# Kernel optimization log

Measured on AMD Instinct MI355X. Metric: run time of the kernel, lower is better.

## Reference

```python
import jax, jax.numpy as jnp
import numpy as np

N, E, IN, H, ED, G, OUT = 50000, 800000, 128, 256, 32, 500, 16
LN_EPS = 1e-5
BN_EPS = 1e-5


def _w(key, shape, scale=0.05):
    return scale * jax.random.normal(key, shape, dtype=jnp.float32)


def setup_inputs() -> dict:
    key = jax.random.key(0)
    ks = iter(jax.random.split(key, 64))
    inp = {
        'x': jax.random.normal(next(ks), (N, IN), jnp.float32),
        'edge_index': jax.random.randint(next(ks), (2, E), 0, N, jnp.int64),
        'edge_attr': jax.random.normal(next(ks), (E, ED), jnp.float32),
        'batch': jnp.sort(jax.random.randint(next(ks), (N,), 0, G, jnp.int64)),
    }
    def conv_params(pfx, din):
        return {
            pfx + '_Wq': _w(next(ks), (din, H)), pfx + '_bq': jnp.zeros((H,), jnp.float32),
            pfx + '_Wk': _w(next(ks), (din, H)), pfx + '_bk': jnp.zeros((H,), jnp.float32),
            pfx + '_Wv': _w(next(ks), (din, H)), pfx + '_bv': jnp.zeros((H,), jnp.float32),
            pfx + '_We': _w(next(ks), (ED, H)),
            pfx + '_Ws': _w(next(ks), (din, H)), pfx + '_bs': jnp.zeros((H,), jnp.float32),
        }
    inp.update(conv_params('conv1', IN))
    inp.update({'ln1_g': jnp.ones((H,), jnp.float32), 'ln1_b': jnp.zeros((H,), jnp.float32)})
    inp.update(conv_params('conv2', H))
    inp.update({'ln2_g': jnp.ones((H,), jnp.float32), 'ln2_b': jnp.zeros((H,), jnp.float32)})
    for pfx in ('gin1', 'gin2'):
        inp.update({
            pfx + '_W1': _w(next(ks), (H, H)), pfx + '_b1': jnp.zeros((H,), jnp.float32),
            pfx + '_bng': jnp.ones((H,), jnp.float32), pfx + '_bnb': jnp.zeros((H,), jnp.float32),
            pfx + '_W2': _w(next(ks), (H, H)), pfx + '_b2': jnp.zeros((H,), jnp.float32),
        })
    inp.update({'lin_W': _w(next(ks), (H, H)), 'lin_b': jnp.zeros((H,), jnp.float32),
                'clf_W': _w(next(ks), (H, OUT)), 'clf_b': jnp.zeros((OUT,), jnp.float32)})
    return inp


def transformer_conv(x, src, dst, ea, Wq, bq, Wk, bk, Wv, bv, We, Ws, bs):
    # PyG TransformerConv, heads=1, edge_dim set, root_weight=True, beta=False
    h = Wq.shape[1]
    q = x @ Wq + bq                      # [N,H]
    e = ea @ We                          # [E,H]
    ke = (x @ Wk + bk)[src] + e          # [E,H]
    ve = (x @ Wv + bv)[src] + e          # [E,H]
    score = jnp.sum(q[dst] * ke, axis=-1) / jnp.sqrt(jnp.float32(h))  # [E]
    m = jax.ops.segment_max(score, dst, num_segments=N)
    ex = jnp.exp(score - m[dst])
    denom = jax.ops.segment_sum(ex, dst, num_segments=N)
    alpha = ex / (denom[dst] + 1e-16)
    out = jax.ops.segment_sum(alpha[:, None] * ve, dst, num_segments=N)
    return out + x @ Ws + bs


def layer_norm(x, g, b):
    mu = jnp.mean(x, axis=-1, keepdims=True)
    var = jnp.var(x, axis=-1, keepdims=True)
    return (x - mu) * jax.lax.rsqrt(var + LN_EPS) * g + b


def gin_conv(x, src, dst, W1, b1, bng, bnb, W2, b2):
    # GINConv(eps=0): mlp(x + sum_{j in N(i)} x_j); MLP = Linear-BN-ReLU-Linear
    agg = jax.ops.segment_sum(x[src], dst, num_segments=N)
    h = x + agg
    y = h @ W1 + b1
    mu = jnp.mean(y, axis=0)
    var = jnp.var(y, axis=0)
    y = (y - mu) * jax.lax.rsqrt(var + BN_EPS) * bng + bnb
    y = jax.nn.relu(y)
    return y @ W2 + b2


def reference(x, edge_index, edge_attr, batch,
              conv1_Wq, conv1_bq, conv1_Wk, conv1_bk, conv1_Wv, conv1_bv, conv1_We, conv1_Ws, conv1_bs,
              ln1_g, ln1_b,
              conv2_Wq, conv2_bq, conv2_Wk, conv2_bk, conv2_Wv, conv2_bv, conv2_We, conv2_Ws, conv2_bs,
              ln2_g, ln2_b,
              gin1_W1, gin1_b1, gin1_bng, gin1_bnb, gin1_W2, gin1_b2,
              gin2_W1, gin2_b1, gin2_bng, gin2_bnb, gin2_W2, gin2_b2,
              lin_W, lin_b, clf_W, clf_b):
    src, dst = edge_index[0], edge_index[1]
    # NodeEncoder (dropout inactive in eval)
    h = transformer_conv(x, src, dst, edge_attr, conv1_Wq, conv1_bq, conv1_Wk, conv1_bk,
                         conv1_Wv, conv1_bv, conv1_We, conv1_Ws, conv1_bs)
    h = layer_norm(jax.nn.leaky_relu(h), ln1_g, ln1_b)
    h = transformer_conv(h, src, dst, edge_attr, conv2_Wq, conv2_bq, conv2_Wk, conv2_bk,
                         conv2_Wv, conv2_bv, conv2_We, conv2_Ws, conv2_bs)
    h = layer_norm(jax.nn.leaky_relu(h), ln2_g, ln2_b)
    # GIN_Net, max_depth=2: conv -> relu -> conv
    h = gin_conv(h, src, dst, gin1_W1, gin1_b1, gin1_bng, gin1_bnb, gin1_W2, gin1_b2)
    h = jax.nn.relu(h)
    h = gin_conv(h, src, dst, gin2_W1, gin2_b1, gin2_bng, gin2_bnb, gin2_W2, gin2_b2)
    # global_add_pool + MLP head
    pooled = jax.ops.segment_sum(h, batch, num_segments=G)   # [G,H]
    z = jax.nn.relu(pooled @ lin_W + lin_b)
    return z @ clf_W + clf_b                                 # [G,OUT]
```

## Files before the change

### kernel.cpp

```cpp
#include <hip/hip_runtime.h>
#include <math.h>

#define NN 50000
#define NE 800000
#define DIN 128
#define DH 256
#define DED 32
#define NG 500
#define DOUT 16
#define SCAN_T 256

typedef __bf16 bf16_t;
typedef __bf16 bf16x4 __attribute__((ext_vector_type(4)));
typedef __bf16 bf16x8 __attribute__((ext_vector_type(8)));
typedef float f32x4 __attribute__((ext_vector_type(4)));

__device__ __forceinline__ void async_copy16(const bf16_t* g, bf16_t* l) {
  __builtin_amdgcn_global_load_lds(
      (const __attribute__((address_space(1))) void*)g,
      (__attribute__((address_space(3))) void*)l, 16, 0, 0);
}

__global__ void fill_i32(int* __restrict__ p, int v, int n) {
  int i = blockIdx.x * 256 + threadIdx.x;
  if (i < n) p[i] = v;
}
__global__ void cast_bf16_k(const float* __restrict__ in, bf16_t* __restrict__ o, long n) {
  long i = (long)blockIdx.x * 256 + threadIdx.x;
  if (i < n) o[i] = (bf16_t)in[i];
}

__global__ void count_k(const int* __restrict__ dst, int* __restrict__ deg) {
  int e = blockIdx.x * 256 + threadIdx.x;
  if (e < NE) atomicAdd(&deg[dst[e]], 1);
}
__global__ void scan1(const int* __restrict__ deg, int* __restrict__ rowptr,
                      int* __restrict__ bsum, int n) {
  __shared__ int s[SCAN_T];
  int t = threadIdx.x, i = blockIdx.x * SCAN_T + t;
  int v = (i < n) ? deg[i] : 0;
  s[t] = v; __syncthreads();
  for (int off = 1; off < SCAN_T; off <<= 1) {
    int add = (t >= off) ? s[t - off] : 0;
    __syncthreads(); s[t] += add; __syncthreads();
  }
  if (i < n) rowptr[i + 1] = s[t];
  if (t == SCAN_T - 1) bsum[blockIdx.x] = s[t];
}
__global__ void scan2(const int* __restrict__ bsum, int* __restrict__ boff, int nb) {
  __shared__ int s[SCAN_T];
  int t = threadIdx.x;
  int v = (t < nb) ? bsum[t] : 0;
  s[t] = v; __syncthreads();
  for (int off = 1; off < SCAN_T; off <<= 1) {
    int add = (t >= off) ? s[t - off] : 0;
    __syncthreads(); s[t] += add; __syncthreads();
  }
  boff[t] = s[t] - v;
}
__global__ void scan3(int* __restrict__ rowptr, const int* __restrict__ boff, int n) {
  int i = blockIdx.x * 256 + threadIdx.x;
  if (i < n) rowptr[i + 1] += boff[i >> 8];
  if (i == 0) rowptr[0] = 0;
}
__global__ void scatter_k(const int* __restrict__ dst, const int* __restrict__ src,
                          const int* __restrict__ rowptr, int* __restrict__ cursor,
                          int* __restrict__ esrc, int* __restrict__ epos) {
  int e = blockIdx.x * 256 + threadIdx.x;
  if (e < NE) {
    int d = dst[e];
    int pos = rowptr[d] + atomicAdd(&cursor[d], 1);
    esrc[pos] = src[e];
    epos[e] = pos;
  }
}
__global__ void permute_ea(const int* __restrict__ epos, const float* __restrict__ ea,
                           bf16_t* __restrict__ eac) {
  long t = (long)blockIdx.x * 256 + threadIdx.x;
  if (t >= (long)NE * 4) return;
  int e = (int)(t >> 2), c8 = ((int)t & 3) * 8;
  int pos = epos[e];
  const float* sp = &ea[(size_t)e * DED + c8];
  bf16x8 o;
#pragma unroll
  for (int j = 0; j < 8; ++j) o[j] = (bf16_t)sp[j];
  *(bf16x8*)&eac[(size_t)pos * DED + c8] = o;
}

struct PackEnt { const float* src; bf16_t* dst; int K; int N; };
struct PackArgs { PackEnt e[16]; };
__global__ void pack_all(PackArgs pa) {
  PackEnt en = pa.e[blockIdx.y];
  int i = blockIdx.x * 256 + threadIdx.x;
  if (i >= en.K * en.N) return;
  int el = i & 511, f = i >> 9;
  int ntiles = en.N >> 4;
  int ks = f / ntiles, t = f - ks * ntiles;
  int lane = el >> 3, j = el & 7;
  int k = ks * 32 + (lane >> 4) * 8 + j;
  int n = t * 16 + (lane & 15);
  en.dst[i] = (bf16_t)en.src[(size_t)k * en.N + n];
}

__global__ void wqe_k(const float* __restrict__ Wq, const float* __restrict__ We,
                      const float* __restrict__ bq, float* __restrict__ Wqe,
                      float* __restrict__ bqe, int din) {
  int idx = blockIdx.x * 256 + threadIdx.x;
  if (idx < din * 32) {
    int d = idx >> 5, j = idx & 31;
    float s = 0.f;
    for (int h = 0; h < DH; ++h) s += Wq[(size_t)d * DH + h] * We[(size_t)j * DH + h];
    Wqe[idx] = s;
  }
  if (idx < 32) {
    float s = 0.f;
    for (int h = 0; h < DH; ++h) s += bq[h] * We[(size_t)idx * DH + h];
    bqe[idx] = s;
  }
}

template<int NT, int RT>
__device__ __forceinline__ void gemm_body(
    const bf16_t* __restrict__ Ab, const bf16_t* __restrict__ Wp,
    const float* __restrict__ bias, float* __restrict__ Cf, bf16_t* __restrict__ Cb,
    int M, int K, int relu, int rstride, int bx,
    float* __restrict__ psum, float* __restrict__ psq)
{
  __shared__ bf16_t Atile[RT * 2048];
  __shared__ bf16_t Btile[NT * 512];
  int tid = threadIdx.x;
  int lane = tid & 63, wv = tid >> 6;
  int base = bx * (RT * 64);
  f32x4 acc[RT][NT];
#pragma unroll
  for (int rt = 0; rt < RT; ++rt)
#pragma unroll
    for (int t = 0; t < NT; ++t) acc[rt][t] = (f32x4){0.f, 0.f, 0.f, 0.f};
  int arow = wv * (16 * RT) + (lane & 15);
  int aq = (lane >> 4) * 8;
  int nk = K >> 5;
  const int ACH = RT * 256;
  const int NCH = ACH + NT * 64;
  for (int ks = 0; ks < nk; ++ks) {
    __syncthreads();
    for (int c = tid; c < NCH; c += 256) {
      if (c < ACH) {
        int r = c >> 2, q = c & 3;
        async_copy16(Ab + (size_t)(base + r) * K + ks * 32 + q * 8, &Atile[c * 8]);
      } else {
        int cb = c - ACH;
        async_copy16(Wp + (size_t)ks * NT * 512 + cb * 8, &Btile[cb * 8]);
      }
    }
    __syncthreads();
    bf16x8 a[RT];
#pragma unroll
    for (int rt = 0; rt < RT; ++rt)
      a[rt] = *(const bf16x8*)&Atile[(arow + rt * 16) * 32 + aq];
#pragma unroll
    for (int t = 0; t < NT; ++t) {
      bf16x8 b = *(const bf16x8*)&Btile[t * 512 + lane * 8];
#pragma unroll
      for (int rt = 0; rt < RT; ++rt)
        acc[rt][t] = __builtin_amdgcn_mfma_f32_16x16x32_bf16(a[rt], b, acc[rt][t], 0, 0, 0);
    }
  }
  int col_l = lane & 15;
#pragma unroll
  for (int rt = 0; rt < RT; ++rt) {
    int rbase = base + wv * (16 * RT) + rt * 16 + (lane >> 4) * 4;
#pragma unroll
    for (int t = 0; t < NT; ++t) {
      int col = t * 16 + col_l;
      float bv = bias ? bias[col] : 0.f;
#pragma unroll
      for (int r = 0; r < 4; ++r) {
        int row = rbase + r;
        if (row >= M) continue;
        float vv = acc[rt][t][r] + bv;
        if (relu) vv = fmaxf(vv, 0.f);
        if (Cf) Cf[(size_t)row * rstride + col] = vv;
        if (Cb) Cb[(size_t)row * rstride + col] = (bf16_t)vv;
      }
    }
  }
  if (psum) {
#pragma unroll
    for (int t = 0; t < NT; ++t) {
      float sc = 0.f, sq = 0.f;
      float bv = bias[t * 16 + col_l];
#pragma unroll
      for (int rt = 0; rt < RT; ++rt) {
        int rbase = base + wv * (16 * RT) + rt * 16 + (lane >> 4) * 4;
#pragma unroll
        for (int r = 0; r < 4; ++r) {
          if (rbase + r >= M) continue;
          float vv = acc[rt][t][r] + bv;
          sc += vv; sq += vv * vv;
        }
      }
      sc += __shfl_xor(sc, 16, 64); sc += __shfl_xor(sc, 32, 64);
      sq += __shfl_xor(sq, 16, 64); sq += __shfl_xor(sq, 32, 64);
      if (lane < 16) {
        int col = t * 16 + lane;
        atomicAdd(&psum[wv * DH + col], sc);
        atomicAdd(&psq[wv * DH + col], sq);
      }
    }
  }
}

template<int NT>
__global__ __launch_bounds__(256, 3) void gemm_r1(
    const bf16_t* __restrict__ Ab, const bf16_t* __restrict__ Wp,
    const float* __restrict__ bias, float* __restrict__ Cf, bf16_t* __restrict__ Cb,
    int M, int K, int relu, int rstride, float* psum, float* psq)
{
  gemm_body<NT, 1>(Ab, Wp, bias, Cf, Cb, M, K, relu, rstride, blockIdx.x, psum, psq);
}

struct QkvsArgs { const bf16_t* w[4]; const float* bias[4]; bf16_t* outp[4]; };
__global__ __launch_bounds__(256, 3) void gemm_qkvs(
    const bf16_t* __restrict__ Ab, QkvsArgs qa, int M, int K)
{
  int which = blockIdx.y;
  gemm_body<16, 2>(Ab, qa.w[which], qa.bias[which], nullptr, qa.outp[which], M, K, 0, 1024,
                   blockIdx.x, nullptr, nullptr);
}

__global__ __launch_bounds__(256) void conv_edge_fused(
    const int* __restrict__ rowptr, const int* __restrict__ esrc,
    const bf16_t* __restrict__ qkvs, const bf16_t* __restrict__ eac,
    const float* __restrict__ QEf,
    bf16_t* __restrict__ AGGn, bf16_t* __restrict__ EAn)
{
  int half = threadIdx.x >> 5, l = threadIdx.x & 31;
  int n = blockIdx.x * 8 + half;
  if (n >= NN) return;
  float q[8];
  {
    bf16x8 t = *(const bf16x8*)&qkvs[(size_t)n * 1024 + l * 8];
#pragma unroll
    for (int j = 0; j < 8; ++j) q[j] = (float)t[j];
  }
  float qe[8];
#pragma unroll
  for (int j = 0; j < 8; ++j) qe[j] = 0.f;
  if (l < 4) {
    const float* p = &QEf[(size_t)n * DED + l * 8];
#pragma unroll
    for (int j = 0; j < 8; ++j) qe[j] = p[j];
  }
  float s = 0.f;
  float acc[8], eacc[8];
#pragma unroll
  for (int j = 0; j < 8; ++j) { acc[j] = 0.f; eacc[j] = 0.f; }
  int i0 = rowptr[n], i1 = rowptr[n + 1];
  for (int wb = i0; wb < i1; wb += 32) {
    int wcnt = min(32, i1 - wb);
    int widx = (l < wcnt) ? esrc[wb + l] : 0;
    int e = 0;
    for (; e + 4 <= wcnt; e += 4) {
      int s1 = __shfl(widx, e, 32);
      int s2 = __shfl(widx, e + 1, 32);
      int s3 = __shfl(widx, e + 2, 32);
      int s4 = __shfl(widx, e + 3, 32);
      const bf16_t* b1 = &qkvs[(size_t)s1 * 1024 + 256 + l * 8];
      const bf16_t* b2 = &qkvs[(size_t)s2 * 1024 + 256 + l * 8];
      const bf16_t* b3 = &qkvs[(size_t)s3 * 1024 + 256 + l * 8];
      const bf16_t* b4 = &qkvs[(size_t)s4 * 1024 + 256 + l * 8];
      bf16x8 k1 = *(const bf16x8*)b1;
      bf16x8 k2 = *(const bf16x8*)b2;
      bf16x8 k3 = *(const bf16x8*)b3;
      bf16x8 k4 = *(const bf16x8*)b4;
      bf16x8 v1 = *(const bf16x8*)(b1 + 256);
      bf16x8 v2 = *(const bf16x8*)(b2 + 256);
      bf16x8 v3 = *(const bf16x8*)(b3 + 256);
      bf16x8 v4 = *(const bf16x8*)(b4 + 256);
      bf16x8 t1 = {}, t2 = {}, t3 = {}, t4 = {};
      if (l < 4) {
        const bf16_t* ep = &eac[(size_t)(wb + e) * DED + l * 8];
        t1 = *(const bf16x8*)ep;
        t2 = *(const bf16x8*)(ep + DED);
        t3 = *(const bf16x8*)(ep + 2 * DED);
        t4 = *(const bf16x8*)(ep + 3 * DED);
      }
      float p1 = 0.f, p2 = 0.f, p3 = 0.f, p4 = 0.f;
#pragma unroll
      for (int j = 0; j < 8; ++j) {
        p1 = fmaf(q[j], (float)k1[j], p1);
        p2 = fmaf(q[j], (float)k2[j], p2);
        p3 = fmaf(q[j], (float)k3[j], p3);
        p4 = fmaf(q[j], (float)k4[j], p4);
      }
#pragma unroll
      for (int j = 0; j < 8; ++j) {
        p1 = fmaf(qe[j], (float)t1[j], p1);
        p2 = fmaf(qe[j], (float)t2[j], p2);
        p3 = fmaf(qe[j], (float)t3[j], p3);
        p4 = fmaf(qe[j], (float)t4[j], p4);
      }
#pragma unroll
      for (int off = 16; off > 0; off >>= 1) {
        p1 += __shfl_xor(p1, off, 64);
        p2 += __shfl_xor(p2, off, 64);
        p3 += __shfl_xor(p3, off, 64);
        p4 += __shfl_xor(p4, off, 64);
      }
      float ex1 = __expf(p1 * 0.0625f);
      float ex2 = __expf(p2 * 0.0625f);
      float ex3 = __expf(p3 * 0.0625f);
      float ex4 = __expf(p4 * 0.0625f);
      s += (ex1 + ex2) + (ex3 + ex4);
#pragma unroll
      for (int j = 0; j < 8; ++j) {
        acc[j] = fmaf(ex1, (float)v1[j], acc[j]);
        acc[j] = fmaf(ex2, (float)v2[j], acc[j]);
        acc[j] = fmaf(ex3, (float)v3[j], acc[j]);
        acc[j] = fmaf(ex4, (float)v4[j], acc[j]);
      }
#pragma unroll
      for (int j = 0; j < 8; ++j) {
        eacc[j] = fmaf(ex1, (float)t1[j], eacc[j]);
        eacc[j] = fmaf(ex2, (float)t2[j], eacc[j]);
        eacc[j] = fmaf(ex3, (float)t3[j], eacc[j]);
        eacc[j] = fmaf(ex4, (float)t4[j], eacc[j]);
      }
    }
    for (; e < wcnt; ++e) {
      int s1 = __shfl(widx, e, 32);
      const bf16_t* b1 = &qkvs[(size_t)s1 * 1024 + 256 + l * 8];
      bf16x8 k1 = *(const bf16x8*)b1;
      bf16x8 v1 = *(const bf16x8*)(b1 + 256);
      bf16x8 t1 = {};
      if (l < 4) t1 = *(const bf16x8*)&eac[(size_t)(wb + e) * DED + l * 8];
      float p1 = 0.f;
#pragma unroll
      for (int j = 0; j < 8; ++j) p1 = fmaf(q[j], (float)k1[j], p1);
#pragma unroll
      for (int j = 0; j < 8; ++j) p1 = fmaf(qe[j], (float)t1[j], p1);
#pragma unroll
      for (int off = 16; off > 0; off >>= 1) p1 += __shfl_xor(p1, off, 64);
      float ex1 = __expf(p1 * 0.0625f);
      s += ex1;
#pragma unroll
      for (int j = 0; j < 8; ++j) acc[j] = fmaf(ex1, (float)v1[j], acc[j]);
#pragma unroll
      for (int j = 0; j < 8; ++j) eacc[j] = fmaf(ex1, (float)t1[j], eacc[j]);
    }
  }
  float inv = 1.f / (s + 1e-16f);
  bf16x8 o;
#pragma unroll
  for (int j = 0; j < 8; ++j) o[j] = (bf16_t)(acc[j] * inv);
  *(bf16x8*)&AGGn[(size_t)n * DH + l * 8] = o;
  if (l < 4) {
    bf16x8 eo;
#pragma unroll
    for (int j = 0; j < 8; ++j) eo[j] = (bf16_t)(eacc[j] * inv);
    *(bf16x8*)&EAn[(size_t)n * DED + l * 8] = eo;
  }
}

__global__ __launch_bounds__(256) void conv_epilogue(
    const bf16_t* __restrict__ AGGn, const bf16_t* __restrict__ E2N,
    const bf16_t* __restrict__ qkvs, const float* __restrict__ g,
    const float* __restrict__ b, bf16_t* __restrict__ out)
{
  int wv = threadIdx.x >> 6, lane = threadIdx.x & 63;
  int n = blockIdx.x * 4 + wv;
  if (n >= NN) return;
  size_t base = (size_t)n * DH + lane * 4;
  bf16x4 a = *(const bf16x4*)&AGGn[base];
  bf16x4 e2 = *(const bf16x4*)&E2N[base];
  bf16x4 sv = *(const bf16x4*)&qkvs[(size_t)n * 1024 + 768 + lane * 4];
  float v[4];
#pragma unroll
  for (int j = 0; j < 4; ++j) {
    float t = (float)a[j] + (float)e2[j] + (float)sv[j];
    v[j] = (t > 0.f) ? t : 0.01f * t;
  }
  float sum = v[0] + v[1] + v[2] + v[3];
  float sq = v[0]*v[0] + v[1]*v[1] + v[2]*v[2] + v[3]*v[3];
#pragma unroll
  for (int off = 32; off > 0; off >>= 1) {
    sum += __shfl_xor(sum, off, 64);
    sq  += __shfl_xor(sq, off, 64);
  }
  float mu = sum * (1.f / DH);
  float var = sq * (1.f / DH) - mu * mu;
  float rstd = rsqrtf(var + 1e-5f);
  bf16x4 o;
#pragma unroll
  for (int j = 0; j < 4; ++j)
    o[j] = (bf16_t)((v[j] - mu) * rstd * g[lane * 4 + j] + b[lane * 4 + j]);
  *(bf16x4*)&out[base] = o;
}

__global__ __launch_bounds__(256) void gin_gather(
    const int* __restrict__ rowptr, const int* __restrict__ esrc,
    const bf16_t* __restrict__ h, bf16_t* __restrict__ out)
{
  int half = threadIdx.x >> 5, l = threadIdx.x & 31;
  int n = blockIdx.x * 8 + half;
  if (n >= NN) return;
  size_t co = (size_t)n * DH + l * 8;
  float acc[8];
  {
    bf16x8 hv = *(const bf16x8*)&h[co];
#pragma unroll
    for (int j = 0; j < 8; ++j) acc[j] = (float)hv[j];
  }
  int i0 = rowptr[n], i1 = rowptr[n + 1];
  for (int wb = i0; wb < i1; wb += 32) {
    int wcnt = min(32, i1 - wb);
    int widx = (l < wcnt) ? esrc[wb + l] : 0;
    int e = 0;
    for (; e + 4 <= wcnt; e += 4) {
      int s1 = __shfl(widx, e, 32);
      int s2 = __shfl(widx, e + 1, 32);
      int s3 = __shfl(widx, e + 2, 32);
      int s4 = __shfl(widx, e + 3, 32);
      bf16x8 t1 = *(const bf16x8*)&h[(size_t)s1 * DH + l * 8];
      bf16x8 t2 = *(const bf16x8*)&h[(size_t)s2 * DH + l * 8];
      bf16x8 t3 = *(const bf16x8*)&h[(size_t)s3 * DH + l * 8];
      bf16x8 t4 = *(const bf16x8*)&h[(size_t)s4 * DH + l * 8];
#pragma unroll
      for (int j = 0; j < 8; ++j)
        acc[j] += ((float)t1[j] + (float)t2[j]) + ((float)t3[j] + (float)t4[j]);
    }
    for (; e < wcnt; ++e) {
      int s1 = __shfl(widx, e, 32);
      bf16x8 t1 = *(const bf16x8*)&h[(size_t)s1 * DH + l * 8];
#pragma unroll
      for (int j = 0; j < 8; ++j) acc[j] += (float)t1[j];
    }
  }
  bf16x8 o;
#pragma unroll
  for (int j = 0; j < 8; ++j) o[j] = (bf16_t)acc[j];
  *(bf16x8*)&out[co] = o;
}

__global__ void bn_final_na(const float* __restrict__ psum, const float* __restrict__ psq,
                            const float* __restrict__ bng, const float* __restrict__ bnb,
                            float* __restrict__ scale, float* __restrict__ shift) {
  int c = threadIdx.x;
  float s = 0.f, ss = 0.f;
  for (int b = 0; b < 4; ++b) { s += psum[b * DH + c]; ss += psq[b * DH + c]; }
  float mu = s * (1.f / NN);
  float var = ss * (1.f / NN) - mu * mu;
  float rstd = rsqrtf(var + 1e-5f);
  float sc = bng[c] * rstd;
  scale[c] = sc;
  shift[c] = bnb[c] - mu * sc;
}
__global__ void bn_apply_relu(const float* __restrict__ y, const float* __restrict__ scale,
                              const float* __restrict__ shift, bf16_t* __restrict__ o, int n) {
  int i = blockIdx.x * 256 + threadIdx.x;
  if (i < n) {
    int c = i & (DH - 1);
    o[i] = (bf16_t)fmaxf(y[i] * scale[c] + shift[c], 0.f);
  }
}

__global__ __launch_bounds__(256) void pool_sorted(
    const int* __restrict__ batch, const float* __restrict__ h, float* __restrict__ pooled)
{
  __shared__ int s0, s1;
  int g = blockIdx.x;
  if (threadIdx.x == 0) {
    int lo = 0, hi = NN;
    while (lo < hi) { int mid = (lo + hi) >> 1; if (batch[mid] < g) lo = mid + 1; else hi = mid; }
    s0 = lo;
  }
  if (threadIdx.x == 1) {
    int lo = 0, hi = NN;
    while (lo < hi) { int mid = (lo + hi) >> 1; if (batch[mid] < g + 1) lo = mid + 1; else hi = mid; }
    s1 = lo;
  }
  __syncthreads();
  int c = threadIdx.x;
  float acc = 0.f;
  for (int r = s0; r < s1; ++r) acc += h[(size_t)r * DH + c];
  pooled[(size_t)g * DH + c] = acc;
}

__global__ __launch_bounds__(256) void gemm_bias_act(
    const float* __restrict__ A, const float* __restrict__ Wm,
    const float* __restrict__ bias, float* __restrict__ C,
    int M, int K, int Ncol, int act)
{
  __shared__ __align__(16) float As[16][68];
  __shared__ __align__(16) float Bs[16][68];
  int tid = threadIdx.x;
  int tx = tid & 15, ty = tid >> 4;
  int row0 = blockIdx.y * 64 + ty * 4;
  int col0 = blockIdx.x * 64 + tx * 4;
  float acc[4][4] = {{0.f}};
  for (int k0 = 0; k0 < K; k0 += 16) {
#pragma unroll
    for (int l = 0; l < 4; ++l) {
      int e = tid + l * 256;
      int r = e >> 4, kk = e & 15;
      int gr = blockIdx.y * 64 + r;
      As[kk][r] = (gr < M) ? A[(size_t)gr * K + k0 + kk] : 0.f;
    }
#pragma unroll
    for (int l = 0; l < 4; ++l) {
      int e = tid + l * 256;
      int kk = e >> 6, c = e & 63;
      int gc = blockIdx.x * 64 + c;
      Bs[kk][c] = (gc < Ncol) ? Wm[(size_t)(k0 + kk) * Ncol + gc] : 0.f;
    }
    __syncthreads();
#pragma unroll
    for (int kk = 0; kk < 16; ++kk) {
      float4 a4 = *(const float4*)&As[kk][ty * 4];
      float4 b4 = *(const float4*)&Bs[kk][tx * 4];
      float a[4] = {a4.x, a4.y, a4.z, a4.w};
      float b[4] = {b4.x, b4.y, b4.z, b4.w};
#pragma unroll
      for (int i = 0; i < 4; ++i)
#pragma unroll
        for (int j = 0; j < 4; ++j)
          acc[i][j] = fmaf(a[i], b[j], acc[i][j]);
    }
    __syncthreads();
  }
#pragma unroll
  for (int i = 0; i < 4; ++i) {
    int r = row0 + i;
    if (r >= M) continue;
#pragma unroll
    for (int j = 0; j < 4; ++j) {
      int c = col0 + j;
      if (c >= Ncol) continue;
      float val = acc[i][j];
      if (bias) val += bias[c];
      if (act == 1) val = fmaxf(val, 0.f);
      C[(size_t)r * Ncol + c] = val;
    }
  }
}

static inline void launch_filli(hipStream_t st, int* p, int v, long n) {
  fill_i32<<<dim3((unsigned)((n + 255) / 256)), dim3(256), 0, st>>>(p, v, (int)n);
}
static inline void launch_cast(hipStream_t st, const float* in, bf16_t* o, long n) {
  cast_bf16_k<<<dim3((unsigned)((n + 255) / 256)), dim3(256), 0, st>>>(in, o, n);
}

extern "C" void kernel_launch(void* const* d_in, const int* in_sizes, int n_in,
                              void* d_out, int out_size, void* d_ws, size_t ws_size,
                              hipStream_t stream) {
  const float* x  = (const float*)d_in[0];
  const int* ei   = (const int*)d_in[1];
  const float* ea = (const float*)d_in[2];
  const int* batch = (const int*)d_in[3];
  const int* src = ei;
  const int* dst = ei + NE;

  const float* c1[9]; for (int i = 0; i < 9; ++i) c1[i] = (const float*)d_in[4 + i];
  const float* ln1g = (const float*)d_in[13]; const float* ln1b = (const float*)d_in[14];
  const float* c2[9]; for (int i = 0; i < 9; ++i) c2[i] = (const float*)d_in[15 + i];
  const float* ln2g = (const float*)d_in[24]; const float* ln2b = (const float*)d_in[25];
  const float* g1[6]; for (int i = 0; i < 6; ++i) g1[i] = (const float*)d_in[26 + i];
  const float* g2[6]; for (int i = 0; i < 6; ++i) g2[i] = (const float*)d_in[32 + i];
  const float* linW = (const float*)d_in[38]; const float* linb = (const float*)d_in[39];
  const float* clfW = (const float*)d_in[40]; const float* clfb = (const float*)d_in[41];
  float* out = (float*)d_out;

  size_t off = 0;
  auto alloc = [&](size_t bytes) -> void* {
    void* r = (char*)d_ws + off;
    off += (bytes + 255) & ~(size_t)255;
    return r;
  };
  int* deg    = (int*)alloc(NN * 4);
  int* cursor = (int*)alloc(NN * 4);
  int* rowptr = (int*)alloc((NN + 1) * 4);
  int* esrc   = (int*)alloc((size_t)NE * 4);
  int* epos   = (int*)alloc((size_t)NE * 4);
  int* bsum   = (int*)alloc(1024);
  int* boff   = (int*)alloc(1024);
  float* QEf   = (float*)alloc((size_t)NN * DED * 4);
  float* Yf    = (float*)alloc((size_t)NN * DH * 4);
  float* pooled = (float*)alloc((size_t)NG * DH * 4);
  float* zbuf   = (float*)alloc((size_t)NG * DH * 4);
  float* psum  = (float*)alloc(4 * DH * 4);
  float* psq   = (float*)alloc(4 * DH * 4);
  float* bnscale = (float*)alloc(DH * 4);
  float* bnshift = (float*)alloc(DH * 4);
  float* wqe_tmp1 = (float*)alloc((size_t)DIN * DED * 4);
  float* wqe_tmp2 = (float*)alloc((size_t)DH * DED * 4);
  float* bqe1 = (float*)alloc(DED * 4);
  float* bqe2 = (float*)alloc(DED * 4);
  bf16_t* qkvsb = (bf16_t*)alloc((size_t)NN * 1024 * 2);
  bf16_t* h_b = (bf16_t*)alloc((size_t)NN * DH * 2);
  bf16_t* g_b = (bf16_t*)alloc((size_t)NN * DH * 2);
  bf16_t* E2Nb = (bf16_t*)alloc((size_t)NN * DH * 2);
  bf16_t* AGGb = (bf16_t*)alloc((size_t)NN * DH * 2);
  bf16_t* EAn = (bf16_t*)alloc((size_t)NN * DED * 2);
  bf16_t* xb  = (bf16_t*)alloc((size_t)NN * DIN * 2);
  bf16_t* eac = (bf16_t*)alloc((size_t)NE * DED * 2);
  float* Hout = (float*)qkvsb;
  bf16_t* pk1q = (bf16_t*)alloc(DIN * DH * 2);
  bf16_t* pk1k = (bf16_t*)alloc(DIN * DH * 2);
  bf16_t* pk1v = (bf16_t*)alloc(DIN * DH * 2);
  bf16_t* pk1s = (bf16_t*)alloc(DIN * DH * 2);
  bf16_t* pk1qe = (bf16_t*)alloc(DIN * DED * 2);
  bf16_t* pk1we = (bf16_t*)alloc(DED * DH * 2);
  bf16_t* pk2q = (bf16_t*)alloc(DH * DH * 2);
  bf16_t* pk2k = (bf16_t*)alloc(DH * DH * 2);
  bf16_t* pk2v = (bf16_t*)alloc(DH * DH * 2);
  bf16_t* pk2s = (bf16_t*)alloc(DH * DH * 2);
  bf16_t* pk2qe = (bf16_t*)alloc(DH * DED * 2);
  bf16_t* pk2we = (bf16_t*)alloc(DED * DH * 2);
  bf16_t* pkg1a = (bf16_t*)alloc(DH * DH * 2);
  bf16_t* pkg1b = (bf16_t*)alloc(DH * DH * 2);
  bf16_t* pkg2a = (bf16_t*)alloc(DH * DH * 2);
  bf16_t* pkg2b = (bf16_t*)alloc(DH * DH * 2);
  if (ws_size < off) return;

  const int GRID_M  = (NN + 127) / 128;
  const int GRID_M1 = (NN + 63) / 64;

  launch_cast(stream, x, xb, (long)NN * DIN);
  wqe_k<<<dim3((DIN * 32 + 255) / 256), dim3(256), 0, stream>>>(c1[0], c1[6], c1[1], wqe_tmp1, bqe1, DIN);
  wqe_k<<<dim3((DH * 32 + 255) / 256), dim3(256), 0, stream>>>(c2[0], c2[6], c2[1], wqe_tmp2, bqe2, DH);
  PackArgs pa;
  pa.e[0]  = {c1[0], pk1q, DIN, DH};
  pa.e[1]  = {c1[2], pk1k, DIN, DH};
  pa.e[2]  = {c1[4], pk1v, DIN, DH};
  pa.e[3]  = {c1[7], pk1s, DIN, DH};
  pa.e[4]  = {c1[6], pk1we, DED, DH};
  pa.e[5]  = {wqe_tmp1, pk1qe, DIN, DED};
  pa.e[6]  = {c2[0], pk2q, DH, DH};
  pa.e[7]  = {c2[2], pk2k, DH, DH};
  pa.e[8]  = {c2[4], pk2v, DH, DH};
  pa.e[9]  = {c2[7], pk2s, DH, DH};
  pa.e[10] = {c2[6], pk2we, DED, DH};
  pa.e[11] = {wqe_tmp2, pk2qe, DH, DED};
  pa.e[12] = {g1[0], pkg1a, DH, DH};
  pa.e[13] = {g1[4], pkg1b, DH, DH};
  pa.e[14] = {g2[0], pkg2a, DH, DH};
  pa.e[15] = {g2[4], pkg2b, DH, DH};
  pack_all<<<dim3(256, 16), dim3(256), 0, stream>>>(pa);

  const int nb1 = (NN + SCAN_T - 1) / SCAN_T;
  launch_filli(stream, deg, 0, NN);
  launch_filli(stream, cursor, 0, NN);
  count_k<<<dim3((NE + 255) / 256), dim3(256), 0, stream>>>(dst, deg);
  scan1<<<dim3(nb1), dim3(SCAN_T), 0, stream>>>(deg, rowptr, bsum, NN);
  scan2<<<dim3(1), dim3(SCAN_T), 0, stream>>>(bsum, boff, nb1);
  scan3<<<dim3(nb1), dim3(SCAN_T), 0, stream>>>(rowptr, boff, NN);
  scatter_k<<<dim3((NE + 255) / 256), dim3(256), 0, stream>>>(dst, src, rowptr, cursor, esrc, epos);
  permute_ea<<<dim3((unsigned)(((long)NE * 4 + 255) / 256)), dim3(256), 0, stream>>>(epos, ea, eac);

  auto conv = [&](const bf16_t* Ain, int K,
                  const bf16_t* pq, const bf16_t* pk, const bf16_t* pv, const bf16_t* ps,
                  const bf16_t* pqe, const bf16_t* pwe,
                  const float* const* P, const float* bqe,
                  const float* lng, const float* lnb, bf16_t* outb) {
    QkvsArgs qa;
    qa.w[0] = pq; qa.w[1] = pk; qa.w[2] = pv; qa.w[3] = ps;
    qa.bias[0] = P[1]; qa.bias[1] = P[3]; qa.bias[2] = P[5]; qa.bias[3] = P[8];
    qa.outp[0] = qkvsb + 0; qa.outp[1] = qkvsb + 256;
    qa.outp[2] = qkvsb + 512; qa.outp[3] = qkvsb + 768;
    gemm_qkvs<<<dim3(GRID_M, 4), dim3(256), 0, stream>>>(Ain, qa, NN, K);
    gemm_r1<2><<<dim3(GRID_M1), dim3(256), 0, stream>>>(
        Ain, pqe, bqe, QEf, nullptr, NN, K, 0, 32, nullptr, nullptr);
    conv_edge_fused<<<dim3((NN + 7) / 8), dim3(256), 0, stream>>>(
        rowptr, esrc, qkvsb, eac, QEf, AGGb, EAn);
    gemm_r1<16><<<dim3(GRID_M1), dim3(256), 0, stream>>>(
        EAn, pwe, nullptr, nullptr, E2Nb, NN, DED, 0, 256, nullptr, nullptr);
    conv_epilogue<<<dim3((NN + 3) / 4), dim3(256), 0, stream>>>(AGGb, E2Nb, qkvsb, lng, lnb, outb);
  };

  auto gin = [&](const bf16_t* hin, const bf16_t* pw1, const bf16_t* pw2,
                 const float* const* P, int relu_out, float* Cf, bf16_t* Cb) {
    gin_gather<<<dim3((NN + 7) / 8), dim3(256), 0, stream>>>(rowptr, esrc, hin, g_b);
    launch_filli(stream, (int*)psum, 0, 2 * 4 * DH);
    gemm_r1<16><<<dim3(GRID_M1), dim3(256), 0, stream>>>(
        g_b, pw1, P[1], Yf, nullptr, NN, DH, 0, 256, psum, psq);
    bn_final_na<<<dim3(1), dim3(256), 0, stream>>>(psum, psq, P[2], P[3], bnscale, bnshift);
    bn_apply_relu<<<dim3((NN * DH + 255) / 256), dim3(256), 0, stream>>>(
        Yf, bnscale, bnshift, g_b, NN * DH);
    gemm_r1<16><<<dim3(GRID_M1), dim3(256), 0, stream>>>(
        g_b, pw2, P[5], Cf, Cb, NN, DH, relu_out, 256, nullptr, nullptr);
  };

  conv(xb, DIN, pk1q, pk1k, pk1v, pk1s, pk1qe, pk1we, c1, bqe1, ln1g, ln1b, h_b);
  conv(h_b, DH, pk2q, pk2k, pk2v, pk2s, pk2qe, pk2we, c2, bqe2, ln2g, ln2b, h_b);
  gin(h_b, pkg1a, pkg1b, g1, 1, nullptr, h_b);
  gin(h_b, pkg2a, pkg2b, g2, 0, Hout, nullptr);

  pool_sorted<<<dim3(NG), dim3(256), 0, stream>>>(batch, Hout, pooled);
  gemm_bias_act<<<dim3(4, 8), dim3(256), 0, stream>>>(pooled, linW, linb, zbuf, NG, DH, DH, 1);
  gemm_bias_act<<<dim3(1, 8), dim3(256), 0, stream>>>(zbuf, clfW, clfb, out, NG, DH, DOUT, 0);
}
```

Measured before the change: 1.358 ms.

## Fuse edge-to-node GEMM with LayerNorm, split gathers across half-waves, use bf16 intermediates

Several changes land together. The E2N GEMM and conv epilogue are merged into one MFMA kernel that applies the residual, leaky-relu and LayerNorm in registers. The edge attention and GIN gather kernels now give each node a full 64-lane wave, with the two 32-lane halves taking alternating edges and their partial sums combined by a cross-half shuffle. The input cast and BN-apply kernels are vectorized to handle 8 elements per thread. The GIN intermediates Y and the final H are stored as bf16 instead of fp32. Together these cut global memory traffic and kernel launches, at the cost of lower precision in Y and H and a heavier per-thread epilogue in the fused GEMM.

After: 1.409 ms. +3.8%, slower.

```diff
diff --git a/kernel.cpp b/kernel.cpp
--- a/kernel.cpp
+++ b/kernel.cpp
@@ -25,9 +25,14 @@
   int i = blockIdx.x * 256 + threadIdx.x;
   if (i < n) p[i] = v;
 }
-__global__ void cast_bf16_k(const float* __restrict__ in, bf16_t* __restrict__ o, long n) {
+__global__ void cast_bf16x8_k(const float* __restrict__ in, bf16_t* __restrict__ o, long n8) {
   long i = (long)blockIdx.x * 256 + threadIdx.x;
-  if (i < n) o[i] = (bf16_t)in[i];
+  if (i >= n8) return;
+  const float* sp = &in[i * 8];
+  bf16x8 r;
+#pragma unroll
+  for (int j = 0; j < 8; ++j) r[j] = (bf16_t)sp[j];
+  *(bf16x8*)&o[i * 8] = r;
 }
 
 __global__ void count_k(const int* __restrict__ dst, int* __restrict__ deg) {
@@ -228,14 +233,88 @@
                    blockIdx.x, nullptr, nullptr);
 }
 
+__global__ __launch_bounds__(256, 3) void gemm_e2n_ln(
+    const bf16_t* __restrict__ Ab, const bf16_t* __restrict__ Wp,
+    const bf16_t* __restrict__ AGG, const bf16_t* __restrict__ qkvs,
+    const float* __restrict__ g, const float* __restrict__ b,
+    bf16_t* __restrict__ out, int M)
+{
+  __shared__ bf16_t Atile[2048];
+  __shared__ bf16_t Btile[16 * 512];
+  int tid = threadIdx.x;
+  int lane = tid & 63, wv = tid >> 6;
+  int base = blockIdx.x * 64;
+  for (int c = tid; c < 256 + 1024; c += 256) {
+    if (c < 256) {
+      int r = c >> 2, q2 = c & 3;
+      async_copy16(Ab + (size_t)(base + r) * 32 + q2 * 8, &Atile[c * 8]);
+    } else {
+      int cb = c - 256;
+      async_copy16(Wp + cb * 8, &Btile[cb * 8]);
+    }
+  }
+  __syncthreads();
+  bf16x8 a0 = *(const bf16x8*)&Atile[(wv * 16 + (lane & 15)) * 32 + (lane >> 4) * 8];
+  f32x4 acc[16];
+#pragma unroll
+  for (int t = 0; t < 16; ++t) {
+    bf16x8 bfr = *(const bf16x8*)&Btile[t * 512 + lane * 8];
+    acc[t] = __builtin_amdgcn_mfma_f32_16x16x32_bf16(a0, bfr, (f32x4){0.f,0.f,0.f,0.f}, 0, 0, 0);
+  }
+  int col_l = lane & 15;
+  int rbase = base + wv * 16 + (lane >> 4) * 4;
+#pragma unroll
+  for (int t = 0; t < 16; ++t) {
+    int col = t * 16 + col_l;
+#pragma unroll
+    for (int r = 0; r < 4; ++r) {
+      int row = rbase + r;
+      float ag = 0.f, sv = 0.f;
+      if (row < M) {
+        ag = (float)AGG[(size_t)row * DH + col];
+        sv = (float)qkvs[(size_t)row * 1024 + 768 + col];
+      }
+      float t1 = acc[t][r] + ag + sv;
+      acc[t][r] = (t1 > 0.f) ? t1 : 0.01f * t1;
+    }
+  }
+  float mu[4], rstd[4];
+#pragma unroll
+  for (int r = 0; r < 4; ++r) {
+    float sum = 0.f, sq = 0.f;
+#pragma unroll
+    for (int t = 0; t < 16; ++t) { sum += acc[t][r]; sq += acc[t][r] * acc[t][r]; }
+#pragma unroll
+    for (int off = 1; off < 16; off <<= 1) {
+      sum += __shfl_xor(sum, off, 16);
+      sq  += __shfl_xor(sq, off, 16);
+    }
+    mu[r] = sum * (1.f / DH);
+    float var = sq * (1.f / DH) - mu[r] * mu[r];
+    rstd[r] = rsqrtf(var + 1e-5f);
+  }
+#pragma unroll
+  for (int t = 0; t < 16; ++t) {
+    int col = t * 16 + col_l;
+    float gc = g[col], bc = b[col];
+#pragma unroll
+    for (int r = 0; r < 4; ++r) {
+      int row = rbase + r;
+      if (row < M)
+        out[(size_t)row * DH + col] = (bf16_t)((acc[t][r] - mu[r]) * rstd[r] * gc + bc);
+    }
+  }
+}
+
 __global__ __launch_bounds__(256) void conv_edge_fused(
     const int* __restrict__ rowptr, const int* __restrict__ esrc,
     const bf16_t* __restrict__ qkvs, const bf16_t* __restrict__ eac,
     const float* __restrict__ QEf,
     bf16_t* __restrict__ AGGn, bf16_t* __restrict__ EAn)
 {
-  int half = threadIdx.x >> 5, l = threadIdx.x & 31;
-  int n = blockIdx.x * 8 + half;
+  int l = threadIdx.x & 31;
+  int half = (threadIdx.x >> 5) & 1;
+  int n = blockIdx.x * 4 + (threadIdx.x >> 6);
   if (n >= NN) return;
   float q[8];
   {
@@ -260,11 +339,11 @@
     int wcnt = min(32, i1 - wb);
     int widx = (l < wcnt) ? esrc[wb + l] : 0;
     int e = 0;
-    for (; e + 4 <= wcnt; e += 4) {
-      int s1 = __shfl(widx, e, 32);
-      int s2 = __shfl(widx, e + 1, 32);
-      int s3 = __shfl(widx, e + 2, 32);
-      int s4 = __shfl(widx, e + 3, 32);
+    for (; e + 8 <= wcnt; e += 8) {
+      int s1 = __shfl(widx, e + half, 32);
+      int s2 = __shfl(widx, e + 2 + half, 32);
+      int s3 = __shfl(widx, e + 4 + half, 32);
+      int s4 = __shfl(widx, e + 6 + half, 32);
       const bf16_t* b1 = &qkvs[(size_t)s1 * 1024 + 256 + l * 8];
       const bf16_t* b2 = &qkvs[(size_t)s2 * 1024 + 256 + l * 8];
       const bf16_t* b3 = &qkvs[(size_t)s3 * 1024 + 256 + l * 8];
@@ -279,11 +358,11 @@
       bf16x8 v4 = *(const bf16x8*)(b4 + 256);
       bf16x8 t1 = {}, t2 = {}, t3 = {}, t4 = {};
       if (l < 4) {
-        const bf16_t* ep = &eac[(size_t)(wb + e) * DED + l * 8];
+        const bf16_t* ep = &eac[(size_t)(wb + e + half) * DED + l * 8];
         t1 = *(const bf16x8*)ep;
-        t2 = *(const bf16x8*)(ep + DED);
-        t3 = *(const bf16x8*)(ep + 2 * DED);
-        t4 = *(const bf16x8*)(ep + 3 * DED);
+        t2 = *(const bf16x8*)(ep + 2 * DED);
+        t3 = *(const bf16x8*)(ep + 4 * DED);
+        t4 = *(const bf16x8*)(ep + 6 * DED);
       }
       float p1 = 0.f, p2 = 0.f, p3 = 0.f, p4 = 0.f;
 #pragma unroll
@@ -302,10 +381,10 @@
       }
 #pragma unroll
       for (int off = 16; off > 0; off >>= 1) {
-        p1 += __shfl_xor(p1, off, 64);
-        p2 += __shfl_xor(p2, off, 64);
-        p3 += __shfl_xor(p3, off, 64);
-        p4 += __shfl_xor(p4, off, 64);
+        p1 += __shfl_xor(p1, off, 32);
+        p2 += __shfl_xor(p2, off, 32);
+        p3 += __shfl_xor(p3, off, 32);
+        p4 += __shfl_xor(p4, off, 32);
       }
       float ex1 = __expf(p1 * 0.0625f);
       float ex2 = __expf(p2 * 0.0625f);
@@ -327,21 +406,23 @@
         eacc[j] = fmaf(ex4, (float)t4[j], eacc[j]);
       }
     }
-    for (; e < wcnt; ++e) {
-      int s1 = __shfl(widx, e, 32);
+    for (; e < wcnt; e += 2) {
+      int eh = e + half;
+      bool act = eh < wcnt;
+      int s1 = __shfl(widx, act ? eh : e, 32);
       const bf16_t* b1 = &qkvs[(size_t)s1 * 1024 + 256 + l * 8];
       bf16x8 k1 = *(const bf16x8*)b1;
       bf16x8 v1 = *(const bf16x8*)(b1 + 256);
       bf16x8 t1 = {};
-      if (l < 4) t1 = *(const bf16x8*)&eac[(size_t)(wb + e) * DED + l * 8];
+      if (act && l < 4) t1 = *(const bf16x8*)&eac[(size_t)(wb + eh) * DED + l * 8];
       float p1 = 0.f;
 #pragma unroll
       for (int j = 0; j < 8; ++j) p1 = fmaf(q[j], (float)k1[j], p1);
 #pragma unroll
       for (int j = 0; j < 8; ++j) p1 = fmaf(qe[j], (float)t1[j], p1);
 #pragma unroll
-      for (int off = 16; off > 0; off >>= 1) p1 += __shfl_xor(p1, off, 64);
-      float ex1 = __expf(p1 * 0.0625f);
+      for (int off = 16; off > 0; off >>= 1) p1 += __shfl_xor(p1, off, 32);
+      float ex1 = act ? __expf(p1 * 0.0625f) : 0.f;
       s += ex1;
 #pragma unroll
       for (int j = 0; j < 8; ++j) acc[j] = fmaf(ex1, (float)v1[j], acc[j]);
@@ -349,78 +430,52 @@
       for (int j = 0; j < 8; ++j) eacc[j] = fmaf(ex1, (float)t1[j], eacc[j]);
     }
   }
+  s += __shfl_xor(s, 32, 64);
+#pragma unroll
+  for (int j = 0; j < 8; ++j) acc[j] += __shfl_xor(acc[j], 32, 64);
+#pragma unroll
+  for (int j = 0; j < 8; ++j) eacc[j] += __shfl_xor(eacc[j], 32, 64);
   float inv = 1.f / (s + 1e-16f);
-  bf16x8 o;
-#pragma unroll
-  for (int j = 0; j < 8; ++j) o[j] = (bf16_t)(acc[j] * inv);
-  *(bf16x8*)&AGGn[(size_t)n * DH + l * 8] = o;
-  if (l < 4) {
-    bf16x8 eo;
-#pragma unroll
-    for (int j = 0; j < 8; ++j) eo[j] = (bf16_t)(eacc[j] * inv);
-    *(bf16x8*)&EAn[(size_t)n * DED + l * 8] = eo;
-  }
-}
-
-__global__ __launch_bounds__(256) void conv_epilogue(
-    const bf16_t* __restrict__ AGGn, const bf16_t* __restrict__ E2N,
-    const bf16_t* __restrict__ qkvs, const float* __restrict__ g,
-    const float* __restrict__ b, bf16_t* __restrict__ out)
-{
-  int wv = threadIdx.x >> 6, lane = threadIdx.x & 63;
-  int n = blockIdx.x * 4 + wv;
-  if (n >= NN) return;
-  size_t base = (size_t)n * DH + lane * 4;
-  bf16x4 a = *(const bf16x4*)&AGGn[base];
-  bf16x4 e2 = *(const bf16x4*)&E2N[base];
-  bf16x4 sv = *(const bf16x4*)&qkvs[(size_t)n * 1024 + 768 + lane * 4];
-  float v[4];
-#pragma unroll
-  for (int j = 0; j < 4; ++j) {
-    float t = (float)a[j] + (float)e2[j] + (float)sv[j];
-    v[j] = (t > 0.f) ? t : 0.01f * t;
-  }
-  float sum = v[0] + v[1] + v[2] + v[3];
-  float sq = v[0]*v[0] + v[1]*v[1] + v[2]*v[2] + v[3]*v[3];
-#pragma unroll
-  for (int off = 32; off > 0; off >>= 1) {
-    sum += __shfl_xor(sum, off, 64);
-    sq  += __shfl_xor(sq, off, 64);
-  }
-  float mu = sum * (1.f / DH);
-  float var = sq * (1.f / DH) - mu * mu;
-  float rstd = rsqrtf(var + 1e-5f);
-  bf16x4 o;
-#pragma unroll
-  for (int j = 0; j < 4; ++j)
-    o[j] = (bf16_t)((v[j] - mu) * rstd * g[lane * 4 + j] + b[lane * 4 + j]);
-  *(bf16x4*)&out[base] = o;
+  if (half == 0) {
+    bf16x8 o;
+#pragma unroll
+    for (int j = 0; j < 8; ++j) o[j] = (bf16_t)(acc[j] * inv);
+    *(bf16x8*)&AGGn[(size_t)n * DH + l * 8] = o;
+    if (l < 4) {
+      bf16x8 eo;
+#pragma unroll
+      for (int j = 0; j < 8; ++j) eo[j] = (bf16_t)(eacc[j] * inv);
+      *(bf16x8*)&EAn[(size_t)n * DED + l * 8] = eo;
+    }
+  }
 }
 
 __global__ __launch_bounds__(256) void gin_gather(
     const int* __restrict__ rowptr, const int* __restrict__ esrc,
     const bf16_t* __restrict__ h, bf16_t* __restrict__ out)
 {
-  int half = threadIdx.x >> 5, l = threadIdx.x & 31;
-  int n = blockIdx.x * 8 + half;
+  int l = threadIdx.x & 31;
+  int half = (threadIdx.x >> 5) & 1;
+  int n = blockIdx.x * 4 + (threadIdx.x >> 6);
   if (n >= NN) return;
   size_t co = (size_t)n * DH + l * 8;
   float acc[8];
   {
     bf16x8 hv = *(const bf16x8*)&h[co];
-#pragma unroll
-    for (int j = 0; j < 8; ++j) acc[j] = (float)hv[j];
+    float w0 = (half == 0) ? 1.f : 0.f;
+#pragma unroll
+    for (int j = 0; j < 8; ++j) acc[j] = w0 * (float)hv[j];
   }
   int i0 = rowptr[n], i1 = rowptr[n + 1];
   for (int wb = i0; wb < i1; wb += 32) {
     int wcnt = min(32, i1 - wb);
     int widx = (l < wcnt) ? esrc[wb + l] : 0;
     int e = 0;
-    for (; e + 4 <= wcnt; e += 4) {
-      int s1 = __shfl(widx, e, 32);
-      int s2 = __shfl(widx, e + 1, 32);
-      int s3 = __shfl(widx, e + 2, 32);
-      int s4 = __shfl(widx, e + 3, 32);
+    for (; e + 8 <= wcnt; e += 8) {
+      int s1 = __shfl(widx, e + half, 32);
+      int s2 = __shfl(widx, e + 2 + half, 32);
+      int s3 = __shfl(widx, e + 4 + half, 32);
+      int s4 = __shfl(widx, e + 6 + half, 32);
       bf16x8 t1 = *(const bf16x8*)&h[(size_t)s1 * DH + l * 8];
       bf16x8 t2 = *(const bf16x8*)&h[(size_t)s2 * DH + l * 8];
       bf16x8 t3 = *(const bf16x8*)&h[(size_t)s3 * DH + l * 8];
@@ -429,17 +484,24 @@
       for (int j = 0; j < 8; ++j)
         acc[j] += ((float)t1[j] + (float)t2[j]) + ((float)t3[j] + (float)t4[j]);
     }
-    for (; e < wcnt; ++e) {
-      int s1 = __shfl(widx, e, 32);
+    for (; e < wcnt; e += 2) {
+      int eh = e + half;
+      bool act = eh < wcnt;
+      int s1 = __shfl(widx, act ? eh : e, 32);
       bf16x8 t1 = *(const bf16x8*)&h[(size_t)s1 * DH + l * 8];
-#pragma unroll
-      for (int j = 0; j < 8; ++j) acc[j] += (float)t1[j];
-    }
-  }
-  bf16x8 o;
-#pragma unroll
-  for (int j = 0; j < 8; ++j) o[j] = (bf16_t)acc[j];
-  *(bf16x8*)&out[co] = o;
+      float w = act ? 1.f : 0.f;
+#pragma unroll
+      for (int j = 0; j < 8; ++j) acc[j] += w * (float)t1[j];
+    }
+  }
+#pragma unroll
+  for (int j = 0; j < 8; ++j) acc[j] += __shfl_xor(acc[j], 32, 64);
+  if (half == 0) {
+    bf16x8 o;
+#pragma unroll
+    for (int j = 0; j < 8; ++j) o[j] = (bf16_t)acc[j];
+    *(bf16x8*)&out[co] = o;
+  }
 }
 
 __global__ void bn_final_na(const float* __restrict__ psum, const float* __restrict__ psq,
@@ -455,17 +517,21 @@
   scale[c] = sc;
   shift[c] = bnb[c] - mu * sc;
 }
-__global__ void bn_apply_relu(const float* __restrict__ y, const float* __restrict__ scale,
-                              const float* __restrict__ shift, bf16_t* __restrict__ o, int n) {
+__global__ void bn_apply_relu8(const bf16_t* __restrict__ y, const float* __restrict__ scale,
+                               const float* __restrict__ shift, bf16_t* __restrict__ o, int n8) {
   int i = blockIdx.x * 256 + threadIdx.x;
-  if (i < n) {
-    int c = i & (DH - 1);
-    o[i] = (bf16_t)fmaxf(y[i] * scale[c] + shift[c], 0.f);
-  }
+  if (i >= n8) return;
+  bf16x8 v = *(const bf16x8*)&y[(size_t)i * 8];
+  int c = (i * 8) & (DH - 1);
+  bf16x8 r;
+#pragma unroll
+  for (int j = 0; j < 8; ++j)
+    r[j] = (bf16_t)fmaxf((float)v[j] * scale[c + j] + shift[c + j], 0.f);
+  *(bf16x8*)&o[(size_t)i * 8] = r;
 }
 
 __global__ __launch_bounds__(256) void pool_sorted(
-    const int* __restrict__ batch, const float* __restrict__ h, float* __restrict__ pooled)
+    const int* __restrict__ batch, const bf16_t* __restrict__ h, float* __restrict__ pooled)
 {
   __shared__ int s0, s1;
   int g = blockIdx.x;
@@ -482,7 +548,7 @@
   __syncthreads();
   int c = threadIdx.x;
   float acc = 0.f;
-  for (int r = s0; r < s1; ++r) acc += h[(size_t)r * DH + c];
+  for (int r = s0; r < s1; ++r) acc += (float)h[(size_t)r * DH + c];
   pooled[(size_t)g * DH + c] = acc;
 }
 
@@ -546,9 +612,6 @@
 
 static inline void launch_filli(hipStream_t st, int* p, int v, long n) {
   fill_i32<<<dim3((unsigned)((n + 255) / 256)), dim3(256), 0, st>>>(p, v, (int)n);
-}
-static inline void launch_cast(hipStream_t st, const float* in, bf16_t* o, long n) {
-  cast_bf16_k<<<dim3((unsigned)((n + 255) / 256)), dim3(256), 0, st>>>(in, o, n);
 }
 
 extern "C" void kernel_launch(void* const* d_in, const int* in_sizes, int n_in,
@@ -585,7 +648,6 @@
   int* bsum   = (int*)alloc(1024);
   int* boff   = (int*)alloc(1024);
   float* QEf   = (float*)alloc((size_t)NN * DED * 4);
-  float* Yf    = (float*)alloc((size_t)NN * DH * 4);
   float* pooled = (float*)alloc((size_t)NG * DH * 4);
   float* zbuf   = (float*)alloc((size_t)NG * DH * 4);
   float* psum  = (float*)alloc(4 * DH * 4);
@@ -599,12 +661,12 @@
   bf16_t* qkvsb = (bf16_t*)alloc((size_t)NN * 1024 * 2);
   bf16_t* h_b = (bf16_t*)alloc((size_t)NN * DH * 2);
   bf16_t* g_b = (bf16_t*)alloc((size_t)NN * DH * 2);
-  bf16_t* E2Nb = (bf16_t*)alloc((size_t)NN * DH * 2);
+  bf16_t* Yb  = (bf16_t*)alloc((size_t)NN * DH * 2);
   bf16_t* AGGb = (bf16_t*)alloc((size_t)NN * DH * 2);
   bf16_t* EAn = (bf16_t*)alloc((size_t)NN * DED * 2);
   bf16_t* xb  = (bf16_t*)alloc((size_t)NN * DIN * 2);
   bf16_t* eac = (bf16_t*)alloc((size_t)NE * DED * 2);
-  float* Hout = (float*)qkvsb;
+  bf16_t* Hb = (bf16_t*)qkvsb;
   bf16_t* pk1q = (bf16_t*)alloc(DIN * DH * 2);
   bf16_t* pk1k = (bf16_t*)alloc(DIN * DH * 2);
   bf16_t* pk1v = (bf16_t*)alloc(DIN * DH * 2);
@@ -626,7 +688,8 @@
   const int GRID_M  = (NN + 127) / 128;
   const int GRID_M1 = (NN + 63) / 64;
 
-  launch_cast(stream, x, xb, (long)NN * DIN);
+  cast_bf16x8_k<<<dim3((unsigned)(((long)NN * DIN / 8 + 255) / 256)), dim3(256), 0, stream>>>(
+      x, xb, (long)NN * DIN / 8);
   wqe_k<<<dim3((DIN * 32 + 255) / 256), dim3(256), 0, stream>>>(c1[0], c1[6], c1[1], wqe_tmp1, bqe1, DIN);
   wqe_k<<<dim3((DH * 32 + 255) / 256), dim3(256), 0, stream>>>(c2[0], c2[6], c2[1], wqe_tmp2, bqe2, DH);
   PackArgs pa;
@@ -671,32 +734,31 @@
     gemm_qkvs<<<dim3(GRID_M, 4), dim3(256), 0, stream>>>(Ain, qa, NN, K);
     gemm_r1<2><<<dim3(GRID_M1), dim3(256), 0, stream>>>(
         Ain, pqe, bqe, QEf, nullptr, NN, K, 0, 32, nullptr, nullptr);
-    conv_edge_fused<<<dim3((NN + 7) / 8), dim3(256), 0, stream>>>(
+    conv_edge_fused<<<dim3((NN + 3) / 4), dim3(256), 0, stream>>>(
         rowptr, esrc, qkvsb, eac, QEf, AGGb, EAn);
-    gemm_r1<16><<<dim3(GRID_M1), dim3(256), 0, stream>>>(
-        EAn, pwe, nullptr, nullptr, E2Nb, NN, DED, 0, 256, nullptr, nullptr);
-    conv_epilogue<<<dim3((NN + 3) / 4), dim3(256), 0, stream>>>(AGGb, E2Nb, qkvsb, lng, lnb, outb);
+    gemm_e2n_ln<<<dim3(GRID_M1), dim3(256), 0, stream>>>(
+        EAn, pwe, AGGb, qkvsb, lng, lnb, outb, NN);
   };
 
   auto gin = [&](const bf16_t* hin, const bf16_t* pw1, const bf16_t* pw2,
-                 const float* const* P, int relu_out, float* Cf, bf16_t* Cb) {
-    gin_gather<<<dim3((NN + 7) / 8), dim3(256), 0, stream>>>(rowptr, esrc, hin, g_b);
+                 const float* const* P, int relu_out, bf16_t* outb) {
+    gin_gather<<<dim3((NN + 3) / 4), dim3(256), 0, stream>>>(rowptr, esrc, hin, g_b);
     launch_filli(stream, (int*)psum, 0, 2 * 4 * DH);
     gemm_r1<16><<<dim3(GRID_M1), dim3(256), 0, stream>>>(
-        g_b, pw1, P[1], Yf, nullptr, NN, DH, 0, 256, psum, psq);
+        g_b, pw1, P[1], nullptr, Yb, NN, DH, 0, 256, psum, psq);
     bn_final_na<<<dim3(1), dim3(256), 0, stream>>>(psum, psq, P[2], P[3], bnscale, bnshift);
-    bn_apply_relu<<<dim3((NN * DH + 255) / 256), dim3(256), 0, stream>>>(
-        Yf, bnscale, bnshift, g_b, NN * DH);
+    bn_apply_relu8<<<dim3((NN * DH / 8 + 255) / 256), dim3(256), 0, stream>>>(
+        Yb, bnscale, bnshift, g_b, NN * DH / 8);
     gemm_r1<16><<<dim3(GRID_M1), dim3(256), 0, stream>>>(
-        g_b, pw2, P[5], Cf, Cb, NN, DH, relu_out, 256, nullptr, nullptr);
+        g_b, pw2, P[5], nullptr, outb, NN, DH, relu_out, 256, nullptr, nullptr);
   };
 
   conv(xb, DIN, pk1q, pk1k, pk1v, pk1s, pk1qe, pk1we, c1, bqe1, ln1g, ln1b, h_b);
   conv(h_b, DH, pk2q, pk2k, pk2v, pk2s, pk2qe, pk2we, c2, bqe2, ln2g, ln2b, h_b);
-  gin(h_b, pkg1a, pkg1b, g1, 1, nullptr, h_b);
-  gin(h_b, pkg2a, pkg2b, g2, 0, Hout, nullptr);
-
-  pool_sorted<<<dim3(NG), dim3(256), 0, stream>>>(batch, Hout, pooled);
+  gin(h_b, pkg1a, pkg1b, g1, 1, h_b);
+  gin(h_b, pkg2a, pkg2b, g2, 0, Hb);
+
+  pool_sorted<<<dim3(NG), dim3(256), 0, stream>>>(batch, Hb, pooled);
   gemm_bias_act<<<dim3(4, 8), dim3(256), 0, stream>>>(pooled, linW, linb, zbuf, NG, DH, DH, 1);
   gemm_bias_act<<<dim3(1, 8), dim3(256), 0, stream>>>(zbuf, clfW, clfb, out, NG, DH, DOUT, 0);
 }
```
